# Optimization experiments

Hardware: AMD Instinct MI355X
Metric: run time of the kernel (lower is better)

## Reference

```python
import jax, jax.numpy as jnp
import numpy as np

B, S, D = 2, 2048, 1024
H, DK = 16, 64
DFF = 4096
WINDOW = 128
GLOBAL = 16
EPS = 1e-5


def _layer_norm(x, g, b):
    mu = jnp.mean(x, axis=-1, keepdims=True)
    var = jnp.var(x, axis=-1, keepdims=True)
    return (x - mu) * jax.lax.rsqrt(var + EPS) * g + b


def setup_inputs() -> dict:
    key = jax.random.key(0)
    ks = jax.random.split(key, 12)
    s = 0.02
    inp = {
        "x": jax.random.normal(ks[0], (B, S, D), dtype=jnp.float32),
        "Wq": jax.random.normal(ks[1], (D, D), jnp.float32) * s,
        "bq": jnp.zeros((D,), jnp.float32),
        "Wk": jax.random.normal(ks[2], (D, D), jnp.float32) * s,
        "bk": jnp.zeros((D,), jnp.float32),
        "Wv": jax.random.normal(ks[3], (D, D), jnp.float32) * s,
        "bv": jnp.zeros((D,), jnp.float32),
        "Wo": jax.random.normal(ks[4], (D, D), jnp.float32) * s,
        "bo": jnp.zeros((D,), jnp.float32),
        "ln1_g": jnp.ones((D,), jnp.float32),
        "ln1_b": jnp.zeros((D,), jnp.float32),
        "W1": jax.random.normal(ks[5], (D, DFF), jnp.float32) * s,
        "b1": jnp.zeros((DFF,), jnp.float32),
        "W2": jax.random.normal(ks[6], (DFF, D), jnp.float32) * s,
        "b2": jnp.zeros((D,), jnp.float32),
        "ln2_g": jnp.ones((D,), jnp.float32),
        "ln2_b": jnp.zeros((D,), jnp.float32),
    }
    return inp


def _local_global_mask(seq_len):
    # token i attends to j iff |i-j| <= WINDOW, or i < GLOBAL, or j < GLOBAL
    i = jnp.arange(seq_len)[:, None]
    j = jnp.arange(seq_len)[None, :]
    m = jnp.abs(i - j) <= WINDOW
    m = m | (i < GLOBAL) | (j < GLOBAL)
    return m  # [S, S] bool


def reference(x, Wq, bq, Wk, bk, Wv, bv, Wo, bo, ln1_g, ln1_b,
              W1, b1, W2, b2, ln2_g, ln2_b):
    # --- self-attention sublayer (pre-norm residual) ---
    xn = _layer_norm(x, ln1_g, ln1_b)
    q = (xn @ Wq + bq).reshape(B, S, H, DK).transpose(0, 2, 1, 3)  # [B,H,S,DK]
    k = (xn @ Wk + bk).reshape(B, S, H, DK).transpose(0, 2, 1, 3)
    v = (xn @ Wv + bv).reshape(B, S, H, DK).transpose(0, 2, 1, 3)

    scores = jnp.einsum('bhqd,bhkd->bhqk', q, k) / jnp.sqrt(jnp.float32(DK))
    mask = _local_global_mask(S)  # [S,S]
    scores = jnp.where(mask[None, None], scores, jnp.float32(-jnp.inf))
    attn = jax.nn.softmax(scores, axis=-1)
    out = jnp.einsum('bhqk,bhkd->bhqd', attn, v)
    out = out.transpose(0, 2, 1, 3).reshape(B, S, D)
    out = out @ Wo + bo
    x = x + out

    # --- feed-forward sublayer (pre-norm residual) ---
    xn2 = _layer_norm(x, ln2_g, ln2_b)
    h = jax.nn.gelu(xn2 @ W1 + b1, approximate=False)
    ff = h @ W2 + b2
    x = x + ff
    return x
```

## Files before the change

### kernel.cpp

```cpp
#include <hip/hip_runtime.h>
#include <stdint.h>


typedef unsigned short u16;
typedef unsigned int   u32;
typedef __attribute__((ext_vector_type(8))) short  short8;
typedef __attribute__((ext_vector_type(4))) float  f32x4;

#define S_LEN   2048
#define D_MODEL 1024
#define ROWS    4096

__device__ __forceinline__ float bf2f(u16 u) {
  union { u32 i; float f; } v; v.i = ((u32)u) << 16; return v.f;
}
__device__ __forceinline__ float bflo(u32 u) {
  union { u32 i; float f; } v; v.i = u << 16; return v.f;
}
__device__ __forceinline__ float bfhi(u32 u) {
  union { u32 i; float f; } v; v.i = u & 0xffff0000u; return v.f;
}
__device__ __forceinline__ u16 f2bf(float f) {
  union { float f; u32 i; } v; v.f = f;
  u32 r = v.i + 0x7fffu + ((v.i >> 16) & 1u);
  return (u16)(r >> 16);
}

__device__ __forceinline__ void gld_lds16(const u16* g, u16* l) {
  __attribute__((address_space(3))) u32* lp =
      reinterpret_cast<__attribute__((address_space(3))) u32*>(
          reinterpret_cast<uintptr_t>(l));
  const __attribute__((address_space(1))) u32* gp =
      reinterpret_cast<const __attribute__((address_space(1))) u32*>(
          reinterpret_cast<uintptr_t>(g));
  __builtin_amdgcn_global_load_lds(gp, lp, 16, 0, 0);
}


#define GBAR  asm volatile("s_barrier" ::: "memory")
#define LGKM(n) asm volatile("s_waitcnt lgkmcnt(" #n ")" ::: "memory")
#define VM(n)   asm volatile("s_waitcnt vmcnt(" #n ")" ::: "memory")
#define SB0   __builtin_amdgcn_sched_barrier(0)

#define STAGE_A(buf, t, hm) do {                                              \
    gld_lds16(pA##hm + (size_t)(t) * 64,      &Ald[buf][0][(hm)*4096 + ldst]);\
    gld_lds16(pA##hm + (size_t)(t) * 64 + 32, &Ald[buf][1][(hm)*4096 + ldst]);\
  } while (0)

#define STAGE_B(buf, t, hm) do {                                              \
    gld_lds16(pB##hm + (size_t)(t) * 64,      &Bld[buf][0][(hm)*4096 + ldst]);\
    gld_lds16(pB##hm + (size_t)(t) * 64 + 32, &Bld[buf][1][(hm)*4096 + ldst]);\
  } while (0)

#define READ_B(buf) do {                                                      \
    _Pragma("unroll") for (int nj = 0; nj < 4; ++nj) {                        \
      bfv[nj][0] = *(const short8*)&Bld[buf][0][brow + nj * 512];             \
      bfv[nj][1] = *(const short8*)&Bld[buf][1][brow + nj * 512]; }           \
  } while (0)

#define READ_A(buf, q) do {                                                   \
    af[(q)&1][0][0] = *(const short8*)&Ald[buf][0][arow + (2*(q)) * 512];     \
    af[(q)&1][0][1] = *(const short8*)&Ald[buf][1][arow + (2*(q)) * 512];     \
    af[(q)&1][1][0] = *(const short8*)&Ald[buf][0][arow + (2*(q)+1) * 512];   \
    af[(q)&1][1][1] = *(const short8*)&Ald[buf][1][arow + (2*(q)+1) * 512];   \
  } while (0)

#define MFMA_Q(q) do {                                                        \
    __builtin_amdgcn_s_setprio(1);                                            \
    _Pragma("unroll") for (int dm = 0; dm < 2; ++dm)                          \
    _Pragma("unroll") for (int kk = 0; kk < 2; ++kk)                          \
    _Pragma("unroll") for (int nj = 0; nj < 4; ++nj)                          \
      acc[2*(q)+dm][nj] = __builtin_amdgcn_mfma_f32_16x16x32_bf16(            \
          af[(q)&1][dm][kk], bfv[nj][kk], acc[2*(q)+dm][nj], 0, 0, 0);        \
    __builtin_amdgcn_s_setprio(0);                                            \
  } while (0)

template <int EPI, int LDK>
__global__ __launch_bounds__(512) void gemm256(
    const u16* __restrict__ A, const u16* __restrict__ Bt,
    const float* __restrict__ bias, u16* __restrict__ C0,
    u16* __restrict__ C1, u16* __restrict__ C2, u16* __restrict__ C3,
    int N, int kc0, int Ktot)
{
  __shared__ __attribute__((aligned(16))) u16 Ald[2][2][256 * 32];
  __shared__ __attribute__((aligned(16))) u16 Bld[2][2][256 * 32];

  const int tid  = threadIdx.x;
  const int w    = tid >> 6;
  const int lane = tid & 63;
  const int wm   = w >> 2;
  const int wn   = w & 3;
  const int lm   = lane & 15;
  const int kq   = lane >> 4;
  const int bm   = blockIdx.y * 256;
  const int bn   = blockIdx.x * 256;
  const int kz   = blockIdx.z;

  const int koff = kz * kc0;
  const int kc   = min(kc0, Ktot - koff);
  const int P    = kc >> 7;

  const u16* Ak = A  + (size_t)koff;
  const u16* Bk = Bt + (size_t)koff;
  u16* C = (kz == 0) ? C0 : (kz == 1) ? C1 : (kz == 2) ? C2 : C3;

  const int rslot = ((kq + (lm >> 1)) & 3) * 8;
  const int arow  = (wm * 128 + lm) * 32 + rslot;
  const int brow  = (wn * 64  + lm) * 32 + rslot;

  const int gcoff = (((lane & 3) - (lane >> 3)) & 3) * 8;
  const int srow  = w * 16 + (lane >> 2);
  const int ldst  = w * 512;

  const u16* pA0 = Ak + (size_t)(bm + srow) * LDK + gcoff;
  const u16* pA1 = pA0 + (size_t)128 * LDK;
  const u16* pB0 = Bk + (size_t)(bn + srow) * LDK + gcoff;
  const u16* pB1 = pB0 + (size_t)128 * LDK;

  f32x4 acc[8][4];
#pragma unroll
  for (int i = 0; i < 8; ++i)
#pragma unroll
    for (int j = 0; j < 4; ++j) acc[i][j] = (f32x4){0.f, 0.f, 0.f, 0.f};

  short8 af[2][2][2];
  short8 bfv[4][2];

  STAGE_B(0, 0, 0); STAGE_B(0, 0, 1);
  STAGE_A(0, 0, 0); STAGE_A(0, 0, 1);
  STAGE_B(1, 1, 0); STAGE_B(1, 1, 1);
  VM(4);
  GBAR;
  READ_A(0, 0);

#pragma unroll 1
  for (int i = 0; i < P - 1; ++i) {
    const int t1 = 2 * i + 1, t2 = 2 * i + 2, t3 = 2 * i + 3;
    GBAR; STAGE_A(1, t1, 0); READ_B(0); READ_A(0, 1); LGKM(4); SB0; MFMA_Q(0);
    GBAR; STAGE_A(1, t1, 1); READ_A(0, 2);            LGKM(4); SB0; MFMA_Q(1);
    GBAR; STAGE_B(0, t2, 0); READ_A(0, 3);            LGKM(4); SB0; MFMA_Q(2);
    VM(2);
    GBAR; STAGE_B(0, t2, 1); READ_A(1, 0);            LGKM(4); SB0; MFMA_Q(3);
    GBAR; STAGE_A(0, t2, 0); READ_B(1); READ_A(1, 1); LGKM(4); SB0; MFMA_Q(0);
    GBAR; STAGE_A(0, t2, 1); READ_A(1, 2);            LGKM(4); SB0; MFMA_Q(1);
    GBAR; STAGE_B(1, t3, 0); READ_A(1, 3);            LGKM(4); SB0; MFMA_Q(2);
    VM(2);
    GBAR; STAGE_B(1, t3, 1); READ_A(0, 0);            LGKM(4); SB0; MFMA_Q(3);
  }
  {
    const int t1 = 2 * P - 1;
    GBAR; STAGE_A(1, t1, 0); READ_B(0); READ_A(0, 1); LGKM(4); SB0; MFMA_Q(0);
    GBAR; STAGE_A(1, t1, 1); READ_A(0, 2);            LGKM(4); SB0; MFMA_Q(1);
    GBAR;                    READ_A(0, 3);            LGKM(4); SB0; MFMA_Q(2);
    VM(0);
    GBAR;                    READ_A(1, 0);            LGKM(4); SB0; MFMA_Q(3);
    GBAR;                    READ_B(1); READ_A(1, 1); LGKM(4); SB0; MFMA_Q(0);
    GBAR;                    READ_A(1, 2);            LGKM(4); SB0; MFMA_Q(1);
    GBAR;                    READ_A(1, 3);            LGKM(4); SB0; MFMA_Q(2);
    LGKM(0); SB0; MFMA_Q(3);
  }

  const int r0 = kq * 4;
#pragma unroll
  for (int mi = 0; mi < 8; ++mi) {
#pragma unroll
    for (int r = 0; r < 4; ++r) {
      const int grow = bm + wm * 128 + mi * 16 + r0 + r;
#pragma unroll
      for (int nj = 0; nj < 4; ++nj) {
        const int gcol = bn + wn * 64 + nj * 16 + lm;
        float v = acc[mi][nj][r];
        if (EPI < 2) v += bias[gcol];
        if (EPI == 1) v = 0.5f * v * (1.0f + erff(v * 0.70710678118654752f));
        C[(size_t)grow * N + gcol] = f2bf(v);
      }
    }
  }
}

__global__ __launch_bounds__(256) void reduce3(
    const u16* __restrict__ P0, const u16* __restrict__ P1,
    const u16* __restrict__ P2,
    const float* __restrict__ bias, const float* res, float* out)
{
  const size_t base = ((size_t)blockIdx.x * 256 + threadIdx.x) * 8;
  const int col = (int)(base & 1023);
  uint4 p0 = *(const uint4*)(P0 + base);
  uint4 p1 = *(const uint4*)(P1 + base);
  uint4 p2 = *(const uint4*)(P2 + base);
  float4 b0 = *(const float4*)(bias + col);
  float4 b1 = *(const float4*)(bias + col + 4);
  float4 r0 = *(const float4*)(res + base);
  float4 r1 = *(const float4*)(res + base + 4);
  float4 o0, o1;
  o0.x = bflo(p0.x) + bflo(p1.x) + bflo(p2.x) + b0.x + r0.x;
  o0.y = bfhi(p0.x) + bfhi(p1.x) + bfhi(p2.x) + b0.y + r0.y;
  o0.z = bflo(p0.y) + bflo(p1.y) + bflo(p2.y) + b0.z + r0.z;
  o0.w = bfhi(p0.y) + bfhi(p1.y) + bfhi(p2.y) + b0.w + r0.w;
  o1.x = bflo(p0.z) + bflo(p1.z) + bflo(p2.z) + b1.x + r1.x;
  o1.y = bfhi(p0.z) + bfhi(p1.z) + bfhi(p2.z) + b1.y + r1.y;
  o1.z = bflo(p0.w) + bflo(p1.w) + bflo(p2.w) + b1.z + r1.z;
  o1.w = bfhi(p0.w) + bfhi(p1.w) + bfhi(p2.w) + b1.w + r1.w;
  *(float4*)(out + base) = o0;
  *(float4*)(out + base + 4) = o1;
}

__global__ __launch_bounds__(256) void reduce4_ln(
    const u16* __restrict__ P0, const u16* __restrict__ P1,
    const u16* __restrict__ P2, const u16* __restrict__ P3,
    const float* __restrict__ bias, const float* __restrict__ res,
    const float* __restrict__ g, const float* __restrict__ bp,
    float* __restrict__ X1, u16* __restrict__ XN)
{
  const int row = blockIdx.x;
  const int t = threadIdx.x;
  const size_t base = (size_t)row * D_MODEL + t * 4;
  const int col = t * 4;
  uint2 a0 = *(const uint2*)(P0 + base);
  uint2 a1 = *(const uint2*)(P1 + base);
  uint2 a2 = *(const uint2*)(P2 + base);
  uint2 a3 = *(const uint2*)(P3 + base);
  float4 bb = *(const float4*)(bias + col);
  float4 rr = *(const float4*)(res + base);
  float4 y;
  y.x = bflo(a0.x) + bflo(a1.x) + bflo(a2.x) + bflo(a3.x) + bb.x + rr.x;
  y.y = bfhi(a0.x) + bfhi(a1.x) + bfhi(a2.x) + bfhi(a3.x) + bb.y + rr.y;
  y.z = bflo(a0.y) + bflo(a1.y) + bflo(a2.y) + bflo(a3.y) + bb.z + rr.z;
  y.w = bfhi(a0.y) + bfhi(a1.y) + bfhi(a2.y) + bfhi(a3.y) + bb.w + rr.w;
  *(float4*)(X1 + base) = y;

  float s  = y.x + y.y + y.z + y.w;
  float ss = y.x * y.x + y.y * y.y + y.z * y.z + y.w * y.w;
#pragma unroll
  for (int off = 32; off > 0; off >>= 1) {
    s  += __shfl_down(s, off);
    ss += __shfl_down(ss, off);
  }
  __shared__ float sm[4], ssm[4], stat[2];
  if ((t & 63) == 0) { sm[t >> 6] = s; ssm[t >> 6] = ss; }
  __syncthreads();
  if (t == 0) {
    float S = sm[0] + sm[1] + sm[2] + sm[3];
    float SS = ssm[0] + ssm[1] + ssm[2] + ssm[3];
    float mu = S * (1.0f / 1024.0f);
    float var = SS * (1.0f / 1024.0f) - mu * mu;
    stat[0] = mu;
    stat[1] = rsqrtf(fmaxf(var, 0.0f) + 1e-5f);
  }
  __syncthreads();
  const float mu = stat[0], rstd = stat[1];
  float4 gg = *(const float4*)(g + col);
  float4 be = *(const float4*)(bp + col);
  u16 o0 = f2bf((y.x - mu) * rstd * gg.x + be.x);
  u16 o1 = f2bf((y.y - mu) * rstd * gg.y + be.y);
  u16 o2 = f2bf((y.z - mu) * rstd * gg.z + be.z);
  u16 o3 = f2bf((y.w - mu) * rstd * gg.w + be.w);
  uint2 wv;
  wv.x = (u32)o0 | ((u32)o1 << 16);
  wv.y = (u32)o2 | ((u32)o3 << 16);
  *(uint2*)(XN + base) = wv;
}

__global__ __launch_bounds__(256) void ln_kernel(
    const float* __restrict__ x, const float* __restrict__ g,
    const float* __restrict__ b, u16* __restrict__ o)
{
  const int row = blockIdx.x;
  const int t = threadIdx.x;
  float4 v = *(const float4*)(x + (size_t)row * D_MODEL + t * 4);
  float s  = v.x + v.y + v.z + v.w;
  float ss = v.x * v.x + v.y * v.y + v.z * v.z + v.w * v.w;
#pragma unroll
  for (int off = 32; off > 0; off >>= 1) {
    s  += __shfl_down(s, off);
    ss += __shfl_down(ss, off);
  }
  __shared__ float sm[4], ssm[4], stat[2];
  if ((t & 63) == 0) { sm[t >> 6] = s; ssm[t >> 6] = ss; }
  __syncthreads();
  if (t == 0) {
    float S = sm[0] + sm[1] + sm[2] + sm[3];
    float SS = ssm[0] + ssm[1] + ssm[2] + ssm[3];
    float mu = S * (1.0f / 1024.0f);
    float var = SS * (1.0f / 1024.0f) - mu * mu;
    stat[0] = mu;
    stat[1] = rsqrtf(fmaxf(var, 0.0f) + 1e-5f);
  }
  __syncthreads();
  const float mu = stat[0], rstd = stat[1];
  float4 gg = *(const float4*)(g + t * 4);
  float4 bb = *(const float4*)(b + t * 4);
  u16 o0 = f2bf((v.x - mu) * rstd * gg.x + bb.x);
  u16 o1 = f2bf((v.y - mu) * rstd * gg.y + bb.y);
  u16 o2 = f2bf((v.z - mu) * rstd * gg.z + bb.z);
  u16 o3 = f2bf((v.w - mu) * rstd * gg.w + bb.w);
  uint2 w;
  w.x = (u32)o0 | ((u32)o1 << 16);
  w.y = (u32)o2 | ((u32)o3 << 16);
  *(uint2*)(o + (size_t)row * D_MODEL + t * 4) = w;
}

__global__ __launch_bounds__(256) void attn_band(
    const u16* __restrict__ qkv, u16* __restrict__ out)
{
  const int t    = threadIdx.x;
  const int w    = t >> 6;
  const int lane = t & 63;
  const int m    = lane & 15;
  const int quad = lane >> 4;
  const int bh   = blockIdx.y;
  const int b    = bh >> 4, h = bh & 15;
  const int i0   = blockIdx.x * 64;
  const size_t bb = (size_t)b * S_LEN;

  __shared__ __attribute__((aligned(16))) u16 Ks[64 * 72];
  __shared__ __attribute__((aligned(16))) u16 Vt[64 * 68];
  __shared__ __attribute__((aligned(16))) u16 Ps[4][16 * 72];

  const u16* qrow = qkv + (bb + i0 + 16 * w + m) * 3072 + h * 64;
  const short8 aq0 = *(const short8*)(qrow + quad * 8);
  const short8 aq1 = *(const short8*)(qrow + 32 + quad * 8);

  f32x4 Ov[4];
#pragma unroll
  for (int td = 0; td < 4; ++td) Ov[td] = (f32x4){0.f, 0.f, 0.f, 0.f};
  float mP[4] = {-1e30f, -1e30f, -1e30f, -1e30f};
  float lS[4] = {0.f, 0.f, 0.f, 0.f};

  const int iB = i0 + 16 * w + quad * 4;

  const int lo = max(64, i0 - 128);
  const int hi = min(S_LEN, i0 + 192);
  const int nChunks = 1 + (hi - lo) / 64;

  const int skr = t >> 2;
  const int skc = (t & 3) * 16;
  const int vkp = (t & 31) * 2;
  const int vd0 = (t >> 5) * 8;

  for (int c = 0; c < nChunks; ++c) {
    const int j0 = (c == 0) ? 0 : lo + (c - 1) * 64;
    __syncthreads();
    {
      const u16* ksrc = qkv + (bb + j0 + skr) * 3072 + 1024 + h * 64 + skc;
      uint4 k0 = *(const uint4*)ksrc;
      uint4 k1 = *(const uint4*)(ksrc + 8);
      *(uint4*)&Ks[skr * 72 + skc]     = k0;
      *(uint4*)&Ks[skr * 72 + skc + 8] = k1;
      const u16* vsrc = qkv + (bb + j0 + vkp) * 3072 + 2048 + h * 64 + vd0;
      uint4 v0 = *(const uint4*)vsrc;
      uint4 v1 = *(const uint4*)(vsrc + 3072);
      const u16 va[8] = {
        (u16)(v0.x & 0xffffu), (u16)(v0.x >> 16),
        (u16)(v0.y & 0xffffu), (u16)(v0.y >> 16),
        (u16)(v0.z & 0xffffu), (u16)(v0.z >> 16),
        (u16)(v0.w & 0xffffu), (u16)(v0.w >> 16)};
      const u16 vb[8] = {
        (u16)(v1.x & 0xffffu), (u16)(v1.x >> 16),
        (u16)(v1.y & 0xffffu), (u16)(v1.y >> 16),
        (u16)(v1.z & 0xffffu), (u16)(v1.z >> 16),
        (u16)(v1.w & 0xffffu), (u16)(v1.w >> 16)};
#pragma unroll
      for (int j = 0; j < 8; ++j)
        *(u32*)&Vt[(vd0 + j) * 68 + vkp] = (u32)va[j] | ((u32)vb[j] << 16);
    }
    __syncthreads();

    f32x4 s[4];
#pragma unroll
    for (int g = 0; g < 4; ++g) {
      const short8 bg0 = *(const short8*)&Ks[(16 * g + m) * 72 + quad * 8];
      const short8 bg1 = *(const short8*)&Ks[(16 * g + m) * 72 + 32 + quad * 8];
      f32x4 sg = (f32x4){0.f, 0.f, 0.f, 0.f};
      sg = __builtin_amdgcn_mfma_f32_16x16x32_bf16(aq0, bg0, sg, 0, 0, 0);
      sg = __builtin_amdgcn_mfma_f32_16x16x32_bf16(aq1, bg1, sg, 0, 0, 0);
      s[g] = sg;
    }

#pragma unroll
    for (int g = 0; g < 4; ++g) {
      const int jG = j0 + 16 * g + m;
#pragma unroll
      for (int r = 0; r < 4; ++r) {
        const int d = iB + r - jG;
        s[g][r] = ((jG < 16) || (d >= -128 && d <= 128)) ? s[g][r] * 0.125f
                                                         : -1e30f;
      }
    }

    float al[4];
#pragma unroll
    for (int r = 0; r < 4; ++r) {
      float mx = fmaxf(fmaxf(s[0][r], s[1][r]), fmaxf(s[2][r], s[3][r]));
      mx = fmaxf(mx, __shfl_xor(mx, 1, 16));
      mx = fmaxf(mx, __shfl_xor(mx, 2, 16));
      mx = fmaxf(mx, __shfl_xor(mx, 4, 16));
      mx = fmaxf(mx, __shfl_xor(mx, 8, 16));
      const float mn = fmaxf(mP[r], mx);
      al[r] = __expf(mP[r] - mn);
      mP[r] = mn;
      const float p0 = __expf(s[0][r] - mn);
      const float p1 = __expf(s[1][r] - mn);
      const float p2 = __expf(s[2][r] - mn);
      const float p3 = __expf(s[3][r] - mn);
      float ps = (p0 + p1) + (p2 + p3);
      ps += __shfl_xor(ps, 1, 16);
      ps += __shfl_xor(ps, 2, 16);
      ps += __shfl_xor(ps, 4, 16);
      ps += __shfl_xor(ps, 8, 16);
      lS[r] = lS[r] * al[r] + ps;
      const int pr = (quad * 4 + r) * 72 + m;
      Ps[w][pr]      = f2bf(p0);
      Ps[w][pr + 16] = f2bf(p1);
      Ps[w][pr + 32] = f2bf(p2);
      Ps[w][pr + 48] = f2bf(p3);
    }
#pragma unroll
    for (int td = 0; td < 4; ++td)
#pragma unroll
      for (int r = 0; r < 4; ++r) Ov[td][r] *= al[r];

    const short8 pa0 = *(const short8*)&Ps[w][m * 72 + quad * 8];
    const short8 pa1 = *(const short8*)&Ps[w][m * 72 + 32 + quad * 8];
#pragma unroll
    for (int td = 0; td < 4; ++td) {
      const short8 bv0 = *(const short8*)&Vt[(td * 16 + m) * 68 + quad * 8];
      const short8 bv1 = *(const short8*)&Vt[(td * 16 + m) * 68 + 32 + quad * 8];
      Ov[td] = __builtin_amdgcn_mfma_f32_16x16x32_bf16(pa0, bv0, Ov[td], 0, 0, 0);
      Ov[td] = __builtin_amdgcn_mfma_f32_16x16x32_bf16(pa1, bv1, Ov[td], 0, 0, 0);
    }
  }

  if (i0 + 16 * w >= 16) {
    float inv[4];
#pragma unroll
    for (int r = 0; r < 4; ++r) inv[r] = 1.0f / lS[r];
#pragma unroll
    for (int td = 0; td < 4; ++td)
#pragma unroll
      for (int r = 0; r < 4; ++r)
        out[(bb + iB + r) * 1024 + h * 64 + td * 16 + m] =
            f2bf(Ov[td][r] * inv[r]);
  }
}

__global__ __launch_bounds__(256) void attn_gpart(
    const u16* __restrict__ qkv, float* __restrict__ Obuf,
    float* __restrict__ mbuf, float* __restrict__ lbuf)
{
  const int t    = threadIdx.x;
  const int w    = t >> 6;
  const int lane = t & 63;
  const int m    = lane & 15;
  const int quad = lane >> 4;
  const int kb   = blockIdx.x;
  const int bh   = blockIdx.y;
  const int b    = bh >> 4, h = bh & 15;
  const size_t bb = (size_t)b * S_LEN;

  __shared__ __attribute__((aligned(16))) u16 Ks[4][32 * 72];
  __shared__ __attribute__((aligned(16))) u16 Vt[4][64 * 40];
  __shared__ __attribute__((aligned(16))) u16 Ps[4][16 * 40];

  const u16* qrow = qkv + (bb + m) * 3072 + h * 64;
  const short8 aq0 = *(const short8*)(qrow + quad * 8);
  const short8 aq1 = *(const short8*)(qrow + 32 + quad * 8);

  f32x4 Ov[4];
#pragma unroll
  for (int td = 0; td < 4; ++td) Ov[td] = (f32x4){0.f, 0.f, 0.f, 0.f};
  float mP[4] = {-1e30f, -1e30f, -1e30f, -1e30f};
  float lS[4] = {0.f, 0.f, 0.f, 0.f};

  const int srow = lane >> 1;
  const int sd   = (lane & 1) * 32;

  for (int c = 0; c < 2; ++c) {
    const int j0 = kb * 256 + w * 64 + c * 32;
    {
      const u16* src = qkv + (bb + j0 + srow) * 3072 + 1024 + h * 64 + sd;
      uint4 k0 = *(const uint4*)(src);
      uint4 k1 = *(const uint4*)(src + 8);
      uint4 k2 = *(const uint4*)(src + 16);
      uint4 k3 = *(const uint4*)(src + 24);
      *(uint4*)&Ks[w][srow * 72 + sd]      = k0;
      *(uint4*)&Ks[w][srow * 72 + sd + 8]  = k1;
      *(uint4*)&Ks[w][srow * 72 + sd + 16] = k2;
      *(uint4*)&Ks[w][srow * 72 + sd + 24] = k3;
#pragma unroll
      for (int q4 = 0; q4 < 4; ++q4) {
        uint4 vv = *(const uint4*)(src + 1024 + q4 * 8);
        const u16 vs[8] = {
          (u16)(vv.x & 0xffffu), (u16)(vv.x >> 16),
          (u16)(vv.y & 0xffffu), (u16)(vv.y >> 16),
          (u16)(vv.z & 0xffffu), (u16)(vv.z >> 16),
          (u16)(vv.w & 0xffffu), (u16)(vv.w >> 16)};
#pragma unroll
        for (int i = 0; i < 8; ++i)
          Vt[w][(sd + q4 * 8 + i) * 40 + srow] = vs[i];
      }
    }

    const short8 b00 = *(const short8*)&Ks[w][m * 72 + quad * 8];
    const short8 b01 = *(const short8*)&Ks[w][m * 72 + 32 + quad * 8];
    const short8 b10 = *(const short8*)&Ks[w][(16 + m) * 72 + quad * 8];
    const short8 b11 = *(const short8*)&Ks[w][(16 + m) * 72 + 32 + quad * 8];
    f32x4 s0 = (f32x4){0.f, 0.f, 0.f, 0.f};
    f32x4 s1 = (f32x4){0.f, 0.f, 0.f, 0.f};
    s0 = __builtin_amdgcn_mfma_f32_16x16x32_bf16(aq0, b00, s0, 0, 0, 0);
    s0 = __builtin_amdgcn_mfma_f32_16x16x32_bf16(aq1, b01, s0, 0, 0, 0);
    s1 = __builtin_amdgcn_mfma_f32_16x16x32_bf16(aq0, b10, s1, 0, 0, 0);
    s1 = __builtin_amdgcn_mfma_f32_16x16x32_bf16(aq1, b11, s1, 0, 0, 0);

    float al[4];
#pragma unroll
    for (int r = 0; r < 4; ++r) {
      const float v0 = s0[r] * 0.125f, v1 = s1[r] * 0.125f;
      float mx = fmaxf(v0, v1);
      mx = fmaxf(mx, __shfl_xor(mx, 1, 16));
      mx = fmaxf(mx, __shfl_xor(mx, 2, 16));
      mx = fmaxf(mx, __shfl_xor(mx, 4, 16));
      mx = fmaxf(mx, __shfl_xor(mx, 8, 16));
      const float mn = fmaxf(mP[r], mx);
      al[r] = __expf(mP[r] - mn);
      mP[r] = mn;
      const float p0 = __expf(v0 - mn);
      const float p1 = __expf(v1 - mn);
      float ps = p0 + p1;
      ps += __shfl_xor(ps, 1, 16);
      ps += __shfl_xor(ps, 2, 16);
      ps += __shfl_xor(ps, 4, 16);
      ps += __shfl_xor(ps, 8, 16);
      lS[r] = lS[r] * al[r] + ps;
      Ps[w][(quad * 4 + r) * 40 + m]      = f2bf(p0);
      Ps[w][(quad * 4 + r) * 40 + 16 + m] = f2bf(p1);
    }
#pragma unroll
    for (int td = 0; td < 4; ++td)
#pragma unroll
      for (int r = 0; r < 4; ++r) Ov[td][r] *= al[r];

    const short8 pa = *(const short8*)&Ps[w][m * 40 + quad * 8];
#pragma unroll
    for (int td = 0; td < 4; ++td) {
      const short8 bv = *(const short8*)&Vt[w][(td * 16 + m) * 40 + quad * 8];
      Ov[td] = __builtin_amdgcn_mfma_f32_16x16x32_bf16(pa, bv, Ov[td], 0, 0, 0);
    }
  }

  const int p = kb * 4 + w;
  const size_t ob = ((size_t)(bh * 32 + p)) * 16 * 64;
#pragma unroll
  for (int td = 0; td < 4; ++td)
#pragma unroll
    for (int r = 0; r < 4; ++r)
      Obuf[ob + (size_t)(quad * 4 + r) * 64 + td * 16 + m] = Ov[td][r];
  if (m == 0) {
    const int mb = (bh * 32 + p) * 16;
#pragma unroll
    for (int r = 0; r < 4; ++r) {
      mbuf[mb + quad * 4 + r] = mP[r];
      lbuf[mb + quad * 4 + r] = lS[r];
    }
  }
}

__global__ __launch_bounds__(256) void attn_gcombine(
    const float* __restrict__ Obuf, const float* __restrict__ mbuf,
    const float* __restrict__ lbuf, u16* __restrict__ out)
{
  const int bh = blockIdx.x;
  const int b  = bh >> 4, h = bh & 15;
  const int t  = threadIdx.x;
  const int q  = t >> 4;
  const int d0 = (t & 15) * 4;
  const int mb = bh * 32 * 16;

  float mv[32];
  float M = -1e30f;
#pragma unroll
  for (int p = 0; p < 32; ++p) {
    mv[p] = mbuf[mb + p * 16 + q];
    M = fmaxf(M, mv[p]);
  }
  float L = 0.f;
  float4 acc = {0.f, 0.f, 0.f, 0.f};
#pragma unroll
  for (int p = 0; p < 32; ++p) {
    const float wp = __expf(mv[p] - M);
    L += lbuf[mb + p * 16 + q] * wp;
    float4 o = *(const float4*)&Obuf[(((size_t)(bh * 32 + p)) * 16 + q) * 64 + d0];
    acc.x += wp * o.x; acc.y += wp * o.y;
    acc.z += wp * o.z; acc.w += wp * o.w;
  }
  const float inv = 1.0f / L;
  uint2 wv;
  wv.x = (u32)f2bf(acc.x * inv) | ((u32)f2bf(acc.y * inv) << 16);
  wv.y = (u32)f2bf(acc.z * inv) | ((u32)f2bf(acc.w * inv) << 16);
  *(uint2*)(out + ((size_t)b * S_LEN + q) * 1024 + h * 64 + d0) = wv;
}

__global__ __launch_bounds__(256) void prep_all(
    const float* __restrict__ Wq, const float* __restrict__ Wk,
    const float* __restrict__ Wv, const float* __restrict__ Wo,
    const float* __restrict__ W1, const float* __restrict__ W2,
    const float* __restrict__ bq, const float* __restrict__ bk,
    const float* __restrict__ bv,
    u16* __restrict__ WQKVT, u16* __restrict__ WOT,
    u16* __restrict__ W1T, u16* __restrict__ W2T,
    float* __restrict__ BQKV)
{
  const int gb = blockIdx.x;
  const int t = threadIdx.x;
  if (gb >= 3072) {
    const int i = (gb - 3072) * 256 + t;
    if (i < 1024) BQKV[i] = bq[i];
    else if (i < 2048) BQKV[i] = bk[i - 1024];
    else BQKV[i] = bv[i - 2048];
    return;
  }
  const float* in; u16* outp; int R, Cc, bx, by;
  if (gb < 1024) {
    const int seg = gb >> 8, local = gb & 255;
    bx = local & 15; by = local >> 4; R = 1024; Cc = 1024;
    in   = (seg == 0) ? Wq : (seg == 1) ? Wk : (seg == 2) ? Wv : Wo;
    outp = (seg < 3) ? WQKVT + (size_t)seg * 1024 * 1024 : WOT;
  } else if (gb < 2048) {
    const int local = gb - 1024;
    bx = local & 63; by = local >> 6; R = 1024; Cc = 4096;
    in = W1; outp = W1T;
  } else {
    const int local = gb - 2048;
    bx = local & 15; by = local >> 4; R = 4096; Cc = 1024;
    in = W2; outp = W2T;
  }

  __shared__ u16 tile[64][65];
  const int tr = by * 64, tc = bx * 64;
  const int lr = t >> 2, lc0 = (t & 3) * 16;
  const float* src = in + (size_t)(tr + lr) * Cc + tc + lc0;
  float4 a0 = *(const float4*)(src);
  float4 a1 = *(const float4*)(src + 4);
  float4 a2 = *(const float4*)(src + 8);
  float4 a3 = *(const float4*)(src + 12);
  const float vals[16] = {a0.x, a0.y, a0.z, a0.w, a1.x, a1.y, a1.z, a1.w,
                          a2.x, a2.y, a2.z, a2.w, a3.x, a3.y, a3.z, a3.w};
#pragma unroll
  for (int q = 0; q < 16; ++q) tile[lr][lc0 + q] = f2bf(vals[q]);
  __syncthreads();
  u16* dst = outp + (size_t)(tc + lr) * R + tr + lc0;
  u32 w[8];
#pragma unroll
  for (int q = 0; q < 8; ++q)
    w[q] = (u32)tile[lc0 + 2 * q][lr] | ((u32)tile[lc0 + 2 * q + 1][lr] << 16);
  uint4 s0; s0.x = w[0]; s0.y = w[1]; s0.z = w[2]; s0.w = w[3];
  uint4 s1; s1.x = w[4]; s1.y = w[5]; s1.z = w[6]; s1.w = w[7];
  *(uint4*)dst = s0;
  *(uint4*)(dst + 8) = s1;
}

static const size_t OFF_WQKVT = 0;
static const size_t OFF_WOT   = OFF_WQKVT + (size_t)3072 * 1024 * 2;
static const size_t OFF_W1T   = OFF_WOT   + (size_t)1024 * 1024 * 2;
static const size_t OFF_W2T   = OFF_W1T   + (size_t)4096 * 1024 * 2;
static const size_t OFF_BQKV  = OFF_W2T   + (size_t)1024 * 4096 * 2;
static const size_t OFF_XN    = OFF_BQKV  + 16384;
static const size_t OFF_QKV   = OFF_XN    + (size_t)4096 * 1024 * 2;
static const size_t OFF_AO    = OFF_QKV   + (size_t)4096 * 3072 * 2;
static const size_t OFF_H     = OFF_QKV;

extern "C" void kernel_launch(void* const* d_in, const int* in_sizes, int n_in,
                              void* d_out, int out_size, void* d_ws, size_t ws_size,
                              hipStream_t stream)
{
  const float* x   = (const float*)d_in[0];
  const float* Wq  = (const float*)d_in[1];
  const float* bq  = (const float*)d_in[2];
  const float* Wk  = (const float*)d_in[3];
  const float* bk  = (const float*)d_in[4];
  const float* Wv  = (const float*)d_in[5];
  const float* bv  = (const float*)d_in[6];
  const float* Wo  = (const float*)d_in[7];
  const float* bo  = (const float*)d_in[8];
  const float* g1  = (const float*)d_in[9];
  const float* be1 = (const float*)d_in[10];
  const float* W1  = (const float*)d_in[11];
  const float* b1  = (const float*)d_in[12];
  const float* W2  = (const float*)d_in[13];
  const float* b2  = (const float*)d_in[14];
  const float* g2  = (const float*)d_in[15];
  const float* be2 = (const float*)d_in[16];
  float* outf = (float*)d_out;
  char* ws = (char*)d_ws;

  u16*   WQKVT = (u16*)(ws + OFF_WQKVT);
  u16*   WOT   = (u16*)(ws + OFF_WOT);
  u16*   W1T   = (u16*)(ws + OFF_W1T);
  u16*   W2T   = (u16*)(ws + OFF_W2T);
  float* BQKV  = (float*)(ws + OFF_BQKV);
  u16*   XN    = (u16*)(ws + OFF_XN);
  u16*   QKV   = (u16*)(ws + OFF_QKV);
  u16*   AO    = (u16*)(ws + OFF_AO);
  u16*   Hbuf  = (u16*)(ws + OFF_H);
  float* X1    = outf;
  u16* PWo0 = (u16*)(ws + OFF_QKV);
  u16* PWo1 = PWo0 + (size_t)4096 * 1024;
  u16* PWo2 = PWo1 + (size_t)4096 * 1024;
  u16* PWo3 = (u16*)(ws + OFF_XN);
  u16* PW20 = (u16*)(ws + OFF_W1T);
  u16* PW21 = (u16*)(ws + OFF_XN);
  u16* PW22 = (u16*)(ws + 0);
  float* GO = (float*)(ws + OFF_XN);
  float* GM = GO + (size_t)32 * 32 * 16 * 64;
  float* GL = GM + 32 * 32 * 16;

  const dim3 blk(256);
  const dim3 blk512(512);
  prep_all<<<dim3(3084), blk, 0, stream>>>(Wq, Wk, Wv, Wo, W1, W2, bq, bk, bv,
                                           WQKVT, WOT, W1T, W2T, BQKV);

  ln_kernel<<<dim3(ROWS), blk, 0, stream>>>(x, g1, be1, XN);
  gemm256<0, 1024><<<dim3(12, 16, 1), blk512, 0, stream>>>(
      XN, WQKVT, BQKV, QKV, QKV, QKV, QKV, 3072, 1024, 1024);
  attn_band<<<dim3(32, 32), blk, 0, stream>>>(QKV, AO);
  attn_gpart<<<dim3(8, 32), blk, 0, stream>>>(QKV, GO, GM, GL);
  attn_gcombine<<<dim3(32), blk, 0, stream>>>(GO, GM, GL, AO);
  gemm256<2, 1024><<<dim3(4, 16, 4), blk512, 0, stream>>>(
      AO, WOT, nullptr, PWo0, PWo1, PWo2, PWo3, 1024, 256, 1024);
  reduce4_ln<<<dim3(ROWS), blk, 0, stream>>>(PWo0, PWo1, PWo2, PWo3,
                                             bo, x, g2, be2, X1, XN);

  gemm256<1, 1024><<<dim3(16, 16, 1), blk512, 0, stream>>>(
      XN, W1T, b1, Hbuf, Hbuf, Hbuf, Hbuf, 4096, 1024, 1024);
  gemm256<2, 4096><<<dim3(4, 16, 3), blk512, 0, stream>>>(
      Hbuf, W2T, nullptr, PW20, PW21, PW22, PW22, 1024, 1536, 4096);
  reduce3<<<dim3(2048), blk, 0, stream>>>(PW20, PW21, PW22, b2, X1, outf);
}
```

Baseline: 336.4 us.

## Widen band-attention query tile, prefetch K/V, and fuse LayerNorm into prep kernel

The band attention kernel now handles 128 query rows per block (two 16-row groups per wave), so each K/V chunk staged in shared memory is reused by twice as many queries. The next chunk's K/V is loaded into registers while the current chunk is computed. The standalone first LayerNorm kernel is folded into the weight-prep launch as extra blocks, removing one launch. In exchange, register pressure rises and the attention grid halves to 512 blocks, and each block scans a wider key range that includes more fully masked chunks.

```diff
diff --git a/kernel.cpp b/kernel.cpp
--- a/kernel.cpp
+++ b/kernel.cpp
@@ -261,45 +261,6 @@
   *(uint2*)(XN + base) = wv;
 }
 
-__global__ __launch_bounds__(256) void ln_kernel(
-    const float* __restrict__ x, const float* __restrict__ g,
-    const float* __restrict__ b, u16* __restrict__ o)
-{
-  const int row = blockIdx.x;
-  const int t = threadIdx.x;
-  float4 v = *(const float4*)(x + (size_t)row * D_MODEL + t * 4);
-  float s  = v.x + v.y + v.z + v.w;
-  float ss = v.x * v.x + v.y * v.y + v.z * v.z + v.w * v.w;
-#pragma unroll
-  for (int off = 32; off > 0; off >>= 1) {
-    s  += __shfl_down(s, off);
-    ss += __shfl_down(ss, off);
-  }
-  __shared__ float sm[4], ssm[4], stat[2];
-  if ((t & 63) == 0) { sm[t >> 6] = s; ssm[t >> 6] = ss; }
-  __syncthreads();
-  if (t == 0) {
-    float S = sm[0] + sm[1] + sm[2] + sm[3];
-    float SS = ssm[0] + ssm[1] + ssm[2] + ssm[3];
-    float mu = S * (1.0f / 1024.0f);
-    float var = SS * (1.0f / 1024.0f) - mu * mu;
-    stat[0] = mu;
-    stat[1] = rsqrtf(fmaxf(var, 0.0f) + 1e-5f);
-  }
-  __syncthreads();
-  const float mu = stat[0], rstd = stat[1];
-  float4 gg = *(const float4*)(g + t * 4);
-  float4 bb = *(const float4*)(b + t * 4);
-  u16 o0 = f2bf((v.x - mu) * rstd * gg.x + bb.x);
-  u16 o1 = f2bf((v.y - mu) * rstd * gg.y + bb.y);
-  u16 o2 = f2bf((v.z - mu) * rstd * gg.z + bb.z);
-  u16 o3 = f2bf((v.w - mu) * rstd * gg.w + bb.w);
-  uint2 w;
-  w.x = (u32)o0 | ((u32)o1 << 16);
-  w.y = (u32)o2 | ((u32)o3 << 16);
-  *(uint2*)(o + (size_t)row * D_MODEL + t * 4) = w;
-}
-
 __global__ __launch_bounds__(256) void attn_band(
     const u16* __restrict__ qkv, u16* __restrict__ out)
 {
@@ -310,27 +271,34 @@
   const int quad = lane >> 4;
   const int bh   = blockIdx.y;
   const int b    = bh >> 4, h = bh & 15;
-  const int i0   = blockIdx.x * 64;
+  const int i0   = blockIdx.x * 128;
   const size_t bb = (size_t)b * S_LEN;
 
   __shared__ __attribute__((aligned(16))) u16 Ks[64 * 72];
   __shared__ __attribute__((aligned(16))) u16 Vt[64 * 68];
-  __shared__ __attribute__((aligned(16))) u16 Ps[4][16 * 72];
-
-  const u16* qrow = qkv + (bb + i0 + 16 * w + m) * 3072 + h * 64;
-  const short8 aq0 = *(const short8*)(qrow + quad * 8);
-  const short8 aq1 = *(const short8*)(qrow + 32 + quad * 8);
-
-  f32x4 Ov[4];
-#pragma unroll
-  for (int td = 0; td < 4; ++td) Ov[td] = (f32x4){0.f, 0.f, 0.f, 0.f};
-  float mP[4] = {-1e30f, -1e30f, -1e30f, -1e30f};
-  float lS[4] = {0.f, 0.f, 0.f, 0.f};
-
-  const int iB = i0 + 16 * w + quad * 4;
+  __shared__ __attribute__((aligned(16))) u16 Ps[4][32 * 72];
+
+  short8 aq0[2], aq1[2];
+#pragma unroll
+  for (int g = 0; g < 2; ++g) {
+    const u16* qrow = qkv + (bb + i0 + 32 * w + 16 * g + m) * 3072 + h * 64;
+    aq0[g] = *(const short8*)(qrow + quad * 8);
+    aq1[g] = *(const short8*)(qrow + 32 + quad * 8);
+  }
+
+  f32x4 Ov[2][4];
+#pragma unroll
+  for (int g = 0; g < 2; ++g)
+#pragma unroll
+    for (int td = 0; td < 4; ++td) Ov[g][td] = (f32x4){0.f, 0.f, 0.f, 0.f};
+  float mP[2][4], lS[2][4];
+#pragma unroll
+  for (int g = 0; g < 2; ++g)
+#pragma unroll
+    for (int r = 0; r < 4; ++r) { mP[g][r] = -1e30f; lS[g][r] = 0.f; }
 
   const int lo = max(64, i0 - 128);
-  const int hi = min(S_LEN, i0 + 192);
+  const int hi = min(S_LEN, i0 + 320);
   const int nChunks = 1 + (hi - lo) / 64;
 
   const int skr = t >> 2;
@@ -338,109 +306,135 @@
   const int vkp = (t & 31) * 2;
   const int vd0 = (t >> 5) * 8;
 
+  uint4 kr0, kr1, vr0, vr1;
+#define LOADKV(j0v) do {                                                      \
+    const u16* ksrc = qkv + (bb + (j0v) + skr) * 3072 + 1024 + h * 64 + skc;  \
+    kr0 = *(const uint4*)ksrc;                                                \
+    kr1 = *(const uint4*)(ksrc + 8);                                          \
+    const u16* vsrc = qkv + (bb + (j0v) + vkp) * 3072 + 2048 + h * 64 + vd0;  \
+    vr0 = *(const uint4*)vsrc;                                                \
+    vr1 = *(const uint4*)(vsrc + 3072);                                       \
+  } while (0)
+
+  LOADKV(0);
+
   for (int c = 0; c < nChunks; ++c) {
-    const int j0 = (c == 0) ? 0 : lo + (c - 1) * 64;
     __syncthreads();
     {
-      const u16* ksrc = qkv + (bb + j0 + skr) * 3072 + 1024 + h * 64 + skc;
-      uint4 k0 = *(const uint4*)ksrc;
-      uint4 k1 = *(const uint4*)(ksrc + 8);
-      *(uint4*)&Ks[skr * 72 + skc]     = k0;
-      *(uint4*)&Ks[skr * 72 + skc + 8] = k1;
-      const u16* vsrc = qkv + (bb + j0 + vkp) * 3072 + 2048 + h * 64 + vd0;
-      uint4 v0 = *(const uint4*)vsrc;
-      uint4 v1 = *(const uint4*)(vsrc + 3072);
+      *(uint4*)&Ks[skr * 72 + skc]     = kr0;
+      *(uint4*)&Ks[skr * 72 + skc + 8] = kr1;
       const u16 va[8] = {
-        (u16)(v0.x & 0xffffu), (u16)(v0.x >> 16),
-        (u16)(v0.y & 0xffffu), (u16)(v0.y >> 16),
-        (u16)(v0.z & 0xffffu), (u16)(v0.z >> 16),
-        (u16)(v0.w & 0xffffu), (u16)(v0.w >> 16)};
+        (u16)(vr0.x & 0xffffu), (u16)(vr0.x >> 16),
+        (u16)(vr0.y & 0xffffu), (u16)(vr0.y >> 16),
+        (u16)(vr0.z & 0xffffu), (u16)(vr0.z >> 16),
+        (u16)(vr0.w & 0xffffu), (u16)(vr0.w >> 16)};
       const u16 vb[8] = {
-        (u16)(v1.x & 0xffffu), (u16)(v1.x >> 16),
-        (u16)(v1.y & 0xffffu), (u16)(v1.y >> 16),
-        (u16)(v1.z & 0xffffu), (u16)(v1.z >> 16),
-        (u16)(v1.w & 0xffffu), (u16)(v1.w >> 16)};
+        (u16)(vr1.x & 0xffffu), (u16)(vr1.x >> 16),
+        (u16)(vr1.y & 0xffffu), (u16)(vr1.y >> 16),
+        (u16)(vr1.z & 0xffffu), (u16)(vr1.z >> 16),
+        (u16)(vr1.w & 0xffffu), (u16)(vr1.w >> 16)};
 #pragma unroll
       for (int j = 0; j < 8; ++j)
         *(u32*)&Vt[(vd0 + j) * 68 + vkp] = (u32)va[j] | ((u32)vb[j] << 16);
     }
     __syncthreads();
 
-    f32x4 s[4];
-#pragma unroll
-    for (int g = 0; g < 4; ++g) {
-      const short8 bg0 = *(const short8*)&Ks[(16 * g + m) * 72 + quad * 8];
-      const short8 bg1 = *(const short8*)&Ks[(16 * g + m) * 72 + 32 + quad * 8];
-      f32x4 sg = (f32x4){0.f, 0.f, 0.f, 0.f};
-      sg = __builtin_amdgcn_mfma_f32_16x16x32_bf16(aq0, bg0, sg, 0, 0, 0);
-      sg = __builtin_amdgcn_mfma_f32_16x16x32_bf16(aq1, bg1, sg, 0, 0, 0);
-      s[g] = sg;
-    }
-
-#pragma unroll
-    for (int g = 0; g < 4; ++g) {
-      const int jG = j0 + 16 * g + m;
+    const int j0 = (c == 0) ? 0 : lo + (c - 1) * 64;
+    if (c + 1 < nChunks) LOADKV(lo + c * 64);
+
+#pragma unroll
+    for (int g = 0; g < 2; ++g) {
+      f32x4 s[4];
+#pragma unroll
+      for (int g4 = 0; g4 < 4; ++g4) {
+        const short8 bg0 = *(const short8*)&Ks[(16 * g4 + m) * 72 + quad * 8];
+        const short8 bg1 =
+            *(const short8*)&Ks[(16 * g4 + m) * 72 + 32 + quad * 8];
+        f32x4 sg = (f32x4){0.f, 0.f, 0.f, 0.f};
+        sg = __builtin_amdgcn_mfma_f32_16x16x32_bf16(aq0[g], bg0, sg, 0, 0, 0);
+        sg = __builtin_amdgcn_mfma_f32_16x16x32_bf16(aq1[g], bg1, sg, 0, 0, 0);
+        s[g4] = sg;
+      }
+      const int iBg = i0 + 32 * w + 16 * g + quad * 4;
+#pragma unroll
+      for (int g4 = 0; g4 < 4; ++g4) {
+        const int jG = j0 + 16 * g4 + m;
+#pragma unroll
+        for (int r = 0; r < 4; ++r) {
+          const int d = iBg + r - jG;
+          s[g4][r] = ((jG < 16) || (d >= -128 && d <= 128))
+                         ? s[g4][r] * 0.125f : -1e30f;
+        }
+      }
+      float al[4];
 #pragma unroll
       for (int r = 0; r < 4; ++r) {
-        const int d = iB + r - jG;
-        s[g][r] = ((jG < 16) || (d >= -128 && d <= 128)) ? s[g][r] * 0.125f
-                                                         : -1e30f;
+        float mx = fmaxf(fmaxf(s[0][r], s[1][r]), fmaxf(s[2][r], s[3][r]));
+        mx = fmaxf(mx, __shfl_xor(mx, 1, 16));
+        mx = fmaxf(mx, __shfl_xor(mx, 2, 16));
+        mx = fmaxf(mx, __shfl_xor(mx, 4, 16));
+        mx = fmaxf(mx, __shfl_xor(mx, 8, 16));
+        const float mn = fmaxf(mP[g][r], mx);
+        al[r] = __expf(mP[g][r] - mn);
+        mP[g][r] = mn;
+        const float p0 = __expf(s[0][r] - mn);
+        const float p1 = __expf(s[1][r] - mn);
+        const float p2 = __expf(s[2][r] - mn);
+        const float p3 = __expf(s[3][r] - mn);
+        float ps = (p0 + p1) + (p2 + p3);
+        ps += __shfl_xor(ps, 1, 16);
+        ps += __shfl_xor(ps, 2, 16);
+        ps += __shfl_xor(ps, 4, 16);
+        ps += __shfl_xor(ps, 8, 16);
+        lS[g][r] = lS[g][r] * al[r] + ps;
+        const int pr = (g * 16 + quad * 4 + r) * 72 + m;
+        Ps[w][pr]      = f2bf(p0);
+        Ps[w][pr + 16] = f2bf(p1);
+        Ps[w][pr + 32] = f2bf(p2);
+        Ps[w][pr + 48] = f2bf(p3);
       }
-    }
-
-    float al[4];
-#pragma unroll
-    for (int r = 0; r < 4; ++r) {
-      float mx = fmaxf(fmaxf(s[0][r], s[1][r]), fmaxf(s[2][r], s[3][r]));
-      mx = fmaxf(mx, __shfl_xor(mx, 1, 16));
-      mx = fmaxf(mx, __shfl_xor(mx, 2, 16));
-      mx = fmaxf(mx, __shfl_xor(mx, 4, 16));
-      mx = fmaxf(mx, __shfl_xor(mx, 8, 16));
-      const float mn = fmaxf(mP[r], mx);
-      al[r] = __expf(mP[r] - mn);
-      mP[r] = mn;
-      const float p0 = __expf(s[0][r] - mn);
-      const float p1 = __expf(s[1][r] - mn);
-      const float p2 = __expf(s[2][r] - mn);
-      const float p3 = __expf(s[3][r] - mn);
-      float ps = (p0 + p1) + (p2 + p3);
-      ps += __shfl_xor(ps, 1, 16);
-      ps += __shfl_xor(ps, 2, 16);
-      ps += __shfl_xor(ps, 4, 16);
-      ps += __shfl_xor(ps, 8, 16);
-      lS[r] = lS[r] * al[r] + ps;
-      const int pr = (quad * 4 + r) * 72 + m;
-      Ps[w][pr]      = f2bf(p0);
-      Ps[w][pr + 16] = f2bf(p1);
-      Ps[w][pr + 32] = f2bf(p2);
-      Ps[w][pr + 48] = f2bf(p3);
-    }
-#pragma unroll
-    for (int td = 0; td < 4; ++td)
-#pragma unroll
-      for (int r = 0; r < 4; ++r) Ov[td][r] *= al[r];
-
-    const short8 pa0 = *(const short8*)&Ps[w][m * 72 + quad * 8];
-    const short8 pa1 = *(const short8*)&Ps[w][m * 72 + 32 + quad * 8];
+#pragma unroll
+      for (int td = 0; td < 4; ++td)
+#pragma unroll
+        for (int r = 0; r < 4; ++r) Ov[g][td][r] *= al[r];
+    }
+
+    short8 pa0[2], pa1[2];
+#pragma unroll
+    for (int g = 0; g < 2; ++g) {
+      pa0[g] = *(const short8*)&Ps[w][(g * 16 + m) * 72 + quad * 8];
+      pa1[g] = *(const short8*)&Ps[w][(g * 16 + m) * 72 + 32 + quad * 8];
+    }
 #pragma unroll
     for (int td = 0; td < 4; ++td) {
       const short8 bv0 = *(const short8*)&Vt[(td * 16 + m) * 68 + quad * 8];
-      const short8 bv1 = *(const short8*)&Vt[(td * 16 + m) * 68 + 32 + quad * 8];
-      Ov[td] = __builtin_amdgcn_mfma_f32_16x16x32_bf16(pa0, bv0, Ov[td], 0, 0, 0);
-      Ov[td] = __builtin_amdgcn_mfma_f32_16x16x32_bf16(pa1, bv1, Ov[td], 0, 0, 0);
-    }
-  }
-
-  if (i0 + 16 * w >= 16) {
-    float inv[4];
-#pragma unroll
-    for (int r = 0; r < 4; ++r) inv[r] = 1.0f / lS[r];
-#pragma unroll
-    for (int td = 0; td < 4; ++td)
-#pragma unroll
-      for (int r = 0; r < 4; ++r)
-        out[(bb + iB + r) * 1024 + h * 64 + td * 16 + m] =
-            f2bf(Ov[td][r] * inv[r]);
+      const short8 bv1 =
+          *(const short8*)&Vt[(td * 16 + m) * 68 + 32 + quad * 8];
+#pragma unroll
+      for (int g = 0; g < 2; ++g) {
+        Ov[g][td] =
+            __builtin_amdgcn_mfma_f32_16x16x32_bf16(pa0[g], bv0, Ov[g][td], 0, 0, 0);
+        Ov[g][td] =
+            __builtin_amdgcn_mfma_f32_16x16x32_bf16(pa1[g], bv1, Ov[g][td], 0, 0, 0);
+      }
+    }
+  }
+#undef LOADKV
+
+#pragma unroll
+  for (int g = 0; g < 2; ++g) {
+    if (i0 + 32 * w + 16 * g >= 16) {
+      const int iBg = i0 + 32 * w + 16 * g + quad * 4;
+      float inv[4];
+#pragma unroll
+      for (int r = 0; r < 4; ++r) inv[r] = 1.0f / lS[g][r];
+#pragma unroll
+      for (int td = 0; td < 4; ++td)
+#pragma unroll
+        for (int r = 0; r < 4; ++r)
+          out[(bb + iBg + r) * 1024 + h * 64 + td * 16 + m] =
+              f2bf(Ov[g][td][r] * inv[r]);
+    }
   }
 }
 
@@ -608,10 +602,49 @@
     const float* __restrict__ bv,
     u16* __restrict__ WQKVT, u16* __restrict__ WOT,
     u16* __restrict__ W1T, u16* __restrict__ W2T,
-    float* __restrict__ BQKV)
+    float* __restrict__ BQKV,
+    const float* __restrict__ x, const float* __restrict__ g1,
+    const float* __restrict__ be1, u16* __restrict__ XN)
 {
   const int gb = blockIdx.x;
   const int t = threadIdx.x;
+  __shared__ u16 tile[64][65];
+  __shared__ float sm[4], ssm[4], stat[2];
+
+  if (gb >= 3084) {
+    const int row = gb - 3084;
+    float4 v = *(const float4*)(x + (size_t)row * D_MODEL + t * 4);
+    float s  = v.x + v.y + v.z + v.w;
+    float ss = v.x * v.x + v.y * v.y + v.z * v.z + v.w * v.w;
+#pragma unroll
+    for (int off = 32; off > 0; off >>= 1) {
+      s  += __shfl_down(s, off);
+      ss += __shfl_down(ss, off);
+    }
+    if ((t & 63) == 0) { sm[t >> 6] = s; ssm[t >> 6] = ss; }
+    __syncthreads();
+    if (t == 0) {
+      float S = sm[0] + sm[1] + sm[2] + sm[3];
+      float SS = ssm[0] + ssm[1] + ssm[2] + ssm[3];
+      float mu = S * (1.0f / 1024.0f);
+      float var = SS * (1.0f / 1024.0f) - mu * mu;
+      stat[0] = mu;
+      stat[1] = rsqrtf(fmaxf(var, 0.0f) + 1e-5f);
+    }
+    __syncthreads();
+    const float mu = stat[0], rstd = stat[1];
+    float4 gg = *(const float4*)(g1 + t * 4);
+    float4 bb = *(const float4*)(be1 + t * 4);
+    u16 o0 = f2bf((v.x - mu) * rstd * gg.x + bb.x);
+    u16 o1 = f2bf((v.y - mu) * rstd * gg.y + bb.y);
+    u16 o2 = f2bf((v.z - mu) * rstd * gg.z + bb.z);
+    u16 o3 = f2bf((v.w - mu) * rstd * gg.w + bb.w);
+    uint2 wv;
+    wv.x = (u32)o0 | ((u32)o1 << 16);
+    wv.y = (u32)o2 | ((u32)o3 << 16);
+    *(uint2*)(XN + (size_t)row * D_MODEL + t * 4) = wv;
+    return;
+  }
   if (gb >= 3072) {
     const int i = (gb - 3072) * 256 + t;
     if (i < 1024) BQKV[i] = bq[i];
@@ -635,7 +668,6 @@
     in = W2; outp = W2T;
   }
 
-  __shared__ u16 tile[64][65];
   const int tr = by * 64, tc = bx * 64;
   const int lr = t >> 2, lc0 = (t & 3) * 16;
   const float* src = in + (size_t)(tr + lr) * Cc + tc + lc0;
@@ -716,13 +748,13 @@
 
   const dim3 blk(256);
   const dim3 blk512(512);
-  prep_all<<<dim3(3084), blk, 0, stream>>>(Wq, Wk, Wv, Wo, W1, W2, bq, bk, bv,
-                                           WQKVT, WOT, W1T, W2T, BQKV);
-
-  ln_kernel<<<dim3(ROWS), blk, 0, stream>>>(x, g1, be1, XN);
+  prep_all<<<dim3(7180), blk, 0, stream>>>(Wq, Wk, Wv, Wo, W1, W2, bq, bk, bv,
+                                           WQKVT, WOT, W1T, W2T, BQKV,
+                                           x, g1, be1, XN);
+
   gemm256<0, 1024><<<dim3(12, 16, 1), blk512, 0, stream>>>(
       XN, WQKVT, BQKV, QKV, QKV, QKV, QKV, 3072, 1024, 1024);
-  attn_band<<<dim3(32, 32), blk, 0, stream>>>(QKV, AO);
+  attn_band<<<dim3(16, 32), blk, 0, stream>>>(QKV, AO);
   attn_gpart<<<dim3(8, 32), blk, 0, stream>>>(QKV, GO, GM, GL);
   attn_gcombine<<<dim3(32), blk, 0, stream>>>(GO, GM, GL, AO);
   gemm256<2, 1024><<<dim3(4, 16, 4), blk512, 0, stream>>>(
```

Result: slower. 345.1 us (+2.6%).
